# Performance work log

Hardware: AMD Instinct MI355X
Metric: run time of the kernel (lower is better)

The kernel has to match this reference:

```python
import jax, jax.numpy as jnp
from jax import lax
import numpy as np

B, S, D = 32, 2048, 512

def setup_inputs() -> dict:
    key = jax.random.key(0)
    ks = jax.random.split(key, 9)
    inv = 1.0 / np.sqrt(D).astype(np.float32)
    return {
        "query": jax.random.normal(ks[0], (B, 1, D), jnp.float32),
        "value": jax.random.normal(ks[1], (B, S, D), jnp.float32),
        "last_alignment_energy": jax.random.uniform(ks[2], (B, S), jnp.float32),
        "conv_w": jax.random.normal(ks[3], (D, 1, 3), jnp.float32) * 0.1,  # Conv1d(1->D,k=3)
        "conv_b": jax.random.normal(ks[4], (D,), jnp.float32) * 0.01,
        "w_q": jax.random.normal(ks[5], (D, D), jnp.float32) * inv,  # applied as x @ w_q
        "w_v": jax.random.normal(ks[6], (D, D), jnp.float32) * inv,
        "bias": jax.random.uniform(ks[7], (D,), jnp.float32, minval=-0.1, maxval=0.1),
        "score_w": jax.random.normal(ks[8], (D,), jnp.float32) * inv,  # score_proj weight (out=1)
        "score_b": jnp.zeros((), jnp.float32),
    }


def reference(query, value, last_alignment_energy, conv_w, conv_b, w_q, w_v, bias, score_w, score_b):
    # location features: Conv1d(1->D, k=3, pad=1) over the previous alignment
    loc = lax.conv_general_dilated(
        last_alignment_energy[:, None, :], conv_w,
        window_strides=(1,), padding=[(1, 1)],
        dimension_numbers=("NCH", "OIH", "NCH"))  # [B, D, S]
    loc = jnp.transpose(loc, (0, 2, 1)) + conv_b  # [B, S, D]

    # additive attention energy: tanh(Wq q + Wv v + loc + b) @ score_w
    hidden = jnp.tanh(query @ w_q + value @ w_v + loc + bias)  # [B, S, D] (query broadcasts over S)
    scores = hidden @ score_w + score_b                          # [B, S]
    align = jax.nn.softmax(scores, axis=-1)                      # [B, S]

    # context = align^T V
    context = jnp.einsum("bs,bsd->bd", align, value)             # [B, D]
    return context, align
```

## Files before the change

### kernel.cpp

```cpp
#include <hip/hip_runtime.h>
#include <hip/hip_bf16.h>

#define B_ 32
#define S_ 2048
#define D_ 512
#define M_ (B_*S_)

typedef __bf16 bf16x8 __attribute__((ext_vector_type(8)));
typedef float  f32x4  __attribute__((ext_vector_type(4)));

__device__ __forceinline__ float tanh_fast(float x){
  float e2 = __expf(2.f * x);
  return 1.f - 2.f * __builtin_amdgcn_rcpf(e2 + 1.f);
}

__global__ void k_reorder_wv(const float* __restrict__ wv,
                             unsigned short* __restrict__ wvr){
  int frag = blockIdx.x;
  int lane = threadIdx.x;
  int ks = frag >> 5, nt = frag & 31;
  int k0 = ks*32 + (lane>>4)*8;
  int d  = nt*16 + (lane&15);
  bf16x8 t;
  #pragma unroll
  for (int j=0;j<8;++j) t[j] = (__bf16)wv[(k0+j)*D_ + d];
  *reinterpret_cast<uint4*>(wvr + ((size_t)frag*64 + lane)*8) =
      __builtin_bit_cast(uint4, t);
}

__global__ void k_qproj(const float* __restrict__ q,
                        const float* __restrict__ wq,
                        const float* __restrict__ bias,
                        float* __restrict__ qp){
  int b  = blockIdx.y;
  int t  = threadIdx.x;
  int dl = t & 127, eg = t >> 7;
  int d  = blockIdx.x*128 + dl;
  __shared__ float qs[D_];
  __shared__ float red[4][128];
  for (int e=t; e<D_; e+=512) qs[e] = q[b*D_+e];
  __syncthreads();
  float acc = 0.f;
  #pragma unroll 8
  for (int i=0;i<128;++i){
    int e = eg*128 + i;
    acc = fmaf(qs[e], wq[(size_t)e*D_+d], acc);
  }
  red[eg][dl] = acc;
  __syncthreads();
  if (eg == 0)
    qp[b*D_+d] = red[0][dl]+red[1][dl]+red[2][dl]+red[3][dl] + bias[d];
}

__launch_bounds__(256, 2)
__global__ void k_energy(const float* __restrict__ value,
                         const unsigned short* __restrict__ wvr,
                         const float* __restrict__ qp,
                         const float* __restrict__ energy,
                         const float* __restrict__ conv_w,
                         const float* __restrict__ conv_b,
                         const float* __restrict__ score_w,
                         float* __restrict__ scores){
  const int t    = threadIdx.x;
  const int wave = t >> 6;
  const int lane = t & 63;
  const int quad = lane >> 4;
  const int lm   = lane & 15;
  const int row0 = blockIdx.x * 64;
  const int b    = row0 >> 11;
  const int s0   = row0 & (S_-1);

  __shared__ __align__(16) unsigned short As[2][4][64][8];

  const int sr  = t >> 2;
  const int so  = t & 3;
  const float* gA = value + (size_t)(row0+sr)*D_ + so*8;
  unsigned short* wA = &As[0][sr>>4][so*16 + (sr&15)][0];

  f32x4 acc[4][8];
  #pragma unroll
  for (int mt=0;mt<4;++mt)
    #pragma unroll
    for (int nt=0;nt<8;++nt)
      acc[mt][nt] = (f32x4){0.f,0.f,0.f,0.f};

  const unsigned short* bP = wvr + ((size_t)(wave*8)*64 + lane)*8;

  {
    f32x4 p0 = *reinterpret_cast<const f32x4*>(gA);
    f32x4 p1 = *reinterpret_cast<const f32x4*>(gA+4);
    bf16x8 tt;
    tt[0]=(__bf16)p0[0]; tt[1]=(__bf16)p0[1]; tt[2]=(__bf16)p0[2]; tt[3]=(__bf16)p0[3];
    tt[4]=(__bf16)p1[0]; tt[5]=(__bf16)p1[1]; tt[6]=(__bf16)p1[2]; tt[7]=(__bf16)p1[3];
    *reinterpret_cast<uint4*>(wA) = __builtin_bit_cast(uint4, tt);
  }
  __syncthreads();

  for (int kc=0; kc<16; ++kc){
    const int buf = kc & 1;
    f32x4 n0, n1;
    if (kc < 15){
      n0 = *reinterpret_cast<const f32x4*>(gA + (kc+1)*32);
      n1 = *reinterpret_cast<const f32x4*>(gA + (kc+1)*32 + 4);
    }
    bf16x8 a[4];
    #pragma unroll
    for (int mt=0;mt<4;++mt)
      a[mt] = *reinterpret_cast<const bf16x8*>(&As[buf][mt][lane][0]);
    bf16x8 bfr[8];
    #pragma unroll
    for (int ntl=0;ntl<8;++ntl)
      bfr[ntl] = __builtin_bit_cast(bf16x8,
        *reinterpret_cast<const uint4*>(bP + (size_t)(kc*32+ntl)*64*8));
    #pragma unroll
    for (int ntl=0;ntl<8;++ntl)
      #pragma unroll
      for (int mt=0;mt<4;++mt)
        acc[mt][ntl] = __builtin_amdgcn_mfma_f32_16x16x32_bf16(a[mt], bfr[ntl], acc[mt][ntl], 0,0,0);
    if (kc < 15){
      bf16x8 tt;
      tt[0]=(__bf16)n0[0]; tt[1]=(__bf16)n0[1]; tt[2]=(__bf16)n0[2]; tt[3]=(__bf16)n0[3];
      tt[4]=(__bf16)n1[0]; tt[5]=(__bf16)n1[1]; tt[6]=(__bf16)n1[2]; tt[7]=(__bf16)n1[3];
      *reinterpret_cast<uint4*>(wA + (buf^1)*2048) = __builtin_bit_cast(uint4, tt);
    }
    __syncthreads();
  }

  float sw[8], c0[8], c1[8], c2[8], cb[8], qv[8];
  #pragma unroll
  for (int ntl=0; ntl<8; ++ntl){
    int d = wave*128 + ntl*16 + lm;
    sw[ntl] = score_w[d];
    c0[ntl] = conv_w[d*3+0];
    c1[ntl] = conv_w[d*3+1];
    c2[ntl] = conv_w[d*3+2];
    cb[ntl] = conv_b[d];
    qv[ntl] = qp[b*D_+d];
  }
  float* red = (float*)&As[0][0][0][0];
  const float* eB = energy + b*S_;
  #pragma unroll
  for (int mt=0; mt<4; ++mt){
    #pragma unroll
    for (int r=0;r<4;++r){
      int sl = mt*16 + quad*4 + r;
      int s  = s0 + sl;
      float em1 = (s > 0)    ? eB[s-1] : 0.f;
      float e0  =              eB[s];
      float ep1 = (s < S_-1) ? eB[s+1] : 0.f;
      float p = 0.f;
      #pragma unroll
      for (int ntl=0; ntl<8; ++ntl){
        float h = acc[mt][ntl][r] + qv[ntl]
                + fmaf(c0[ntl],em1, fmaf(c1[ntl],e0, fmaf(c2[ntl],ep1, cb[ntl])));
        p = fmaf(sw[ntl], tanh_fast(h), p);
      }
      #pragma unroll
      for (int m=1; m<16; m<<=1) p += __shfl_xor(p, m, 64);
      if (lm == 0) red[wave*64 + sl] = p;
    }
  }
  __syncthreads();
  if (t < 64)
    scores[row0 + t] = red[t] + red[64+t] + red[128+t] + red[192+t];
}

__global__ void k_softmax(const float* __restrict__ sp,
                          const float* __restrict__ score_b,
                          float* __restrict__ out_align){
  int b = blockIdx.x, t = threadIdx.x;
  int lane = t & 63, wid = t >> 6;
  float sb = score_b[0];
  float v[8], mx = -3.4e38f;
  #pragma unroll
  for (int i=0;i<8;++i){
    float sc = sp[b*S_ + t + i*256] + sb;
    v[i] = sc;
    mx = fmaxf(mx, sc);
  }
  __shared__ float red[4], red2[4];
  #pragma unroll
  for (int m=1;m<64;m<<=1) mx = fmaxf(mx, __shfl_xor(mx, m, 64));
  if (lane==0) red[wid] = mx;
  __syncthreads();
  mx = fmaxf(fmaxf(red[0],red[1]), fmaxf(red[2],red[3]));
  float sum = 0.f;
  #pragma unroll
  for (int i=0;i<8;++i){ v[i] = __expf(v[i]-mx); sum += v[i]; }
  #pragma unroll
  for (int m=1;m<64;m<<=1) sum += __shfl_xor(sum, m, 64);
  if (lane==0) red2[wid] = sum;
  __syncthreads();
  sum = red2[0]+red2[1]+red2[2]+red2[3];
  float inv = 1.f/sum;
  #pragma unroll
  for (int i=0;i<8;++i) out_align[b*S_ + t + i*256] = v[i]*inv;
}

__global__ void k_ctx_part(const float* __restrict__ value,
                           const float* __restrict__ align,
                           float* __restrict__ cpart){
  int b = blockIdx.y, sc = blockIdx.x;
  int t = threadIdx.x;
  int r = t >> 7;
  int c = (t & 127) * 4;
  f32x4 acc = (f32x4){0.f,0.f,0.f,0.f};
  for (int i=0;i<64;++i){
    int s = sc*128 + i*2 + r;
    float al = align[b*S_+s];
    f32x4 v = *reinterpret_cast<const f32x4*>(value + ((size_t)(b*S_+s))*D_ + c);
    acc += al * v;
  }
  __shared__ float lred[2][D_];
  #pragma unroll
  for (int j=0;j<4;++j) lred[r][c+j] = acc[j];
  __syncthreads();
  if (r == 0){
    #pragma unroll
    for (int j=0;j<4;++j)
      cpart[((size_t)(b*16+sc))*D_ + c + j] = lred[0][c+j] + lred[1][c+j];
  }
}

__global__ void k_ctx_reduce(const float* __restrict__ cpart,
                             float* __restrict__ out_ctx){
  int idx = blockIdx.x*256 + threadIdx.x;
  int b = idx >> 9, d = idx & 511;
  float s = 0.f;
  #pragma unroll
  for (int j=0;j<16;++j) s += cpart[((size_t)(b*16+j))*D_ + d];
  out_ctx[idx] = s;
}

extern "C" void kernel_launch(void* const* d_in, const int* in_sizes, int n_in,
                              void* d_out, int out_size, void* d_ws, size_t ws_size,
                              hipStream_t stream){
  const float* query   = (const float*)d_in[0];
  const float* value   = (const float*)d_in[1];
  const float* energy  = (const float*)d_in[2];
  const float* conv_w  = (const float*)d_in[3];
  const float* conv_b  = (const float*)d_in[4];
  const float* w_q     = (const float*)d_in[5];
  const float* w_v     = (const float*)d_in[6];
  const float* bias    = (const float*)d_in[7];
  const float* score_w = (const float*)d_in[8];
  const float* score_b = (const float*)d_in[9];

  char* ws = (char*)d_ws;
  unsigned short* wvr = (unsigned short*)(ws);
  float* qp    = (float*)(ws + (512<<10));
  float* sp    = (float*)(ws + (576<<10));
  float* cpart = (float*)(ws + (832<<10));

  float* out_ctx   = (float*)d_out;
  float* out_align = out_ctx + B_*D_;

  k_reorder_wv<<<dim3(512),      dim3(64),  0, stream>>>(w_v, wvr);
  k_qproj     <<<dim3(4,32),     dim3(512), 0, stream>>>(query, w_q, bias, qp);
  k_energy    <<<dim3(M_/64),    dim3(256), 0, stream>>>(value, wvr, qp, energy,
                                                         conv_w, conv_b, score_w, sp);
  k_softmax   <<<dim3(B_),       dim3(256), 0, stream>>>(sp, score_b, out_align);
  k_ctx_part  <<<dim3(16,B_),    dim3(256), 0, stream>>>(value, out_align, cpart);
  k_ctx_reduce<<<dim3(B_*D_/256),dim3(256), 0, stream>>>(cpart, out_ctx);
}
```

Before: 287.3 us.

## Retile energy GEMM to 128x256 blocks with LDS-staged weights and split columns

The energy GEMM now gives each block 128 rows and half of the D columns. The two column halves write partial scores that the softmax kernel sums. Weight fragments are staged into LDS with global_load_lds and shared by the waves, instead of each wave reading them from global memory. This raises reuse of both A and B tiles, at the cost of value rows being read twice, once per column half. The ctx partial kernel now uses 512 threads with four row groups, which adds parallelism in the context reduction.

Measured after the change: 289.0 us. About the same (+0.6%).

```diff
diff --git a/kernel.cpp b/kernel.cpp
--- a/kernel.cpp
+++ b/kernel.cpp
@@ -12,6 +12,19 @@
 __device__ __forceinline__ float tanh_fast(float x){
   float e2 = __expf(2.f * x);
   return 1.f - 2.f * __builtin_amdgcn_rcpf(e2 + 1.f);
+}
+
+__device__ __forceinline__ void gl_lds16(const void* g, void* l){
+  __builtin_amdgcn_global_load_lds(
+      (const __attribute__((address_space(1))) unsigned int*)g,
+      (__attribute__((address_space(3))) unsigned int*)l, 16, 0, 0);
+}
+
+__device__ __forceinline__ bf16x8 cvt8(f32x4 a, f32x4 b){
+  bf16x8 t;
+  t[0]=(__bf16)a[0]; t[1]=(__bf16)a[1]; t[2]=(__bf16)a[2]; t[3]=(__bf16)a[3];
+  t[4]=(__bf16)b[0]; t[5]=(__bf16)b[1]; t[6]=(__bf16)b[2]; t[7]=(__bf16)b[3];
+  return t;
 }
 
 __global__ void k_reorder_wv(const float* __restrict__ wv,
@@ -60,22 +73,28 @@
                          const float* __restrict__ conv_w,
                          const float* __restrict__ conv_b,
                          const float* __restrict__ score_w,
-                         float* __restrict__ scores){
+                         float* __restrict__ scores_part){
   const int t    = threadIdx.x;
   const int wave = t >> 6;
   const int lane = t & 63;
   const int quad = lane >> 4;
   const int lm   = lane & 15;
-  const int row0 = blockIdx.x * 64;
+  const int wh   = wave & 1;
+  const int wc   = wave >> 1;
+
+  const int rowtile = blockIdx.x >> 1;
+  const int colh    = blockIdx.x & 1;
+  const int row0 = rowtile * 128;
   const int b    = row0 >> 11;
   const int s0   = row0 & (S_-1);
 
-  __shared__ __align__(16) unsigned short As[2][4][64][8];
-
-  const int sr  = t >> 2;
-  const int so  = t & 3;
-  const float* gA = value + (size_t)(row0+sr)*D_ + so*8;
-  unsigned short* wA = &As[0][sr>>4][so*16 + (sr&15)][0];
+  __shared__ __align__(16) unsigned short As[2][4096];
+  __shared__ __align__(16) unsigned short Bs[2][8192];
+
+  const int bmt = t >> 6, bo = (t >> 4) & 3;
+  const int blm = t & 15;
+  const float* gA1 = value + (size_t)(row0 + bmt*16 + blm)*D_ + bo*8;
+  const float* gA2 = gA1 + (size_t)64*D_;
 
   f32x4 acc[4][8];
   #pragma unroll
@@ -84,44 +103,57 @@
     for (int nt=0;nt<8;++nt)
       acc[mt][nt] = (f32x4){0.f,0.f,0.f,0.f};
 
-  const unsigned short* bP = wvr + ((size_t)(wave*8)*64 + lane)*8;
-
   {
-    f32x4 p0 = *reinterpret_cast<const f32x4*>(gA);
-    f32x4 p1 = *reinterpret_cast<const f32x4*>(gA+4);
-    bf16x8 tt;
-    tt[0]=(__bf16)p0[0]; tt[1]=(__bf16)p0[1]; tt[2]=(__bf16)p0[2]; tt[3]=(__bf16)p0[3];
-    tt[4]=(__bf16)p1[0]; tt[5]=(__bf16)p1[1]; tt[6]=(__bf16)p1[2]; tt[7]=(__bf16)p1[3];
-    *reinterpret_cast<uint4*>(wA) = __builtin_bit_cast(uint4, tt);
+    #pragma unroll
+    for (int i=0;i<4;++i){
+      int lf = wave*4 + i;
+      int frag = 0*32 + colh*16 + lf;
+      gl_lds16((const char*)wvr + (size_t)frag*1024 + lane*16,
+               (char*)&Bs[0][0] + lf*1024);
+    }
+    f32x4 p0 = *reinterpret_cast<const f32x4*>(gA1);
+    f32x4 p1 = *reinterpret_cast<const f32x4*>(gA1+4);
+    f32x4 p2 = *reinterpret_cast<const f32x4*>(gA2);
+    f32x4 p3 = *reinterpret_cast<const f32x4*>(gA2+4);
+    *reinterpret_cast<uint4*>(&As[0][(size_t)t*8])       = __builtin_bit_cast(uint4, cvt8(p0,p1));
+    *reinterpret_cast<uint4*>(&As[0][(size_t)(t+256)*8]) = __builtin_bit_cast(uint4, cvt8(p2,p3));
   }
   __syncthreads();
 
   for (int kc=0; kc<16; ++kc){
     const int buf = kc & 1;
-    f32x4 n0, n1;
     if (kc < 15){
-      n0 = *reinterpret_cast<const f32x4*>(gA + (kc+1)*32);
-      n1 = *reinterpret_cast<const f32x4*>(gA + (kc+1)*32 + 4);
+      #pragma unroll
+      for (int i=0;i<4;++i){
+        int lf = wave*4 + i;
+        int frag = (kc+1)*32 + colh*16 + lf;
+        gl_lds16((const char*)wvr + (size_t)frag*1024 + lane*16,
+                 (char*)&Bs[buf^1][0] + lf*1024);
+      }
+    }
+    f32x4 n0,n1,n2,n3;
+    if (kc < 15){
+      n0 = *reinterpret_cast<const f32x4*>(gA1 + (kc+1)*32);
+      n1 = *reinterpret_cast<const f32x4*>(gA1 + (kc+1)*32 + 4);
+      n2 = *reinterpret_cast<const f32x4*>(gA2 + (kc+1)*32);
+      n3 = *reinterpret_cast<const f32x4*>(gA2 + (kc+1)*32 + 4);
     }
     bf16x8 a[4];
     #pragma unroll
     for (int mt=0;mt<4;++mt)
-      a[mt] = *reinterpret_cast<const bf16x8*>(&As[buf][mt][lane][0]);
-    bf16x8 bfr[8];
-    #pragma unroll
-    for (int ntl=0;ntl<8;++ntl)
-      bfr[ntl] = __builtin_bit_cast(bf16x8,
-        *reinterpret_cast<const uint4*>(bP + (size_t)(kc*32+ntl)*64*8));
-    #pragma unroll
-    for (int ntl=0;ntl<8;++ntl)
+      a[mt] = *reinterpret_cast<const bf16x8*>(
+                &As[buf][(size_t)(((wh*4+mt)*64 + quad*16 + lm))*8]);
+    #pragma unroll
+    for (int ntl=0;ntl<8;++ntl){
+      bf16x8 bf = *reinterpret_cast<const bf16x8*>(
+                    &Bs[buf][(size_t)((wc*8+ntl)*64 + lane)*8]);
       #pragma unroll
       for (int mt=0;mt<4;++mt)
-        acc[mt][ntl] = __builtin_amdgcn_mfma_f32_16x16x32_bf16(a[mt], bfr[ntl], acc[mt][ntl], 0,0,0);
+        acc[mt][ntl] = __builtin_amdgcn_mfma_f32_16x16x32_bf16(a[mt], bf, acc[mt][ntl], 0,0,0);
+    }
     if (kc < 15){
-      bf16x8 tt;
-      tt[0]=(__bf16)n0[0]; tt[1]=(__bf16)n0[1]; tt[2]=(__bf16)n0[2]; tt[3]=(__bf16)n0[3];
-      tt[4]=(__bf16)n1[0]; tt[5]=(__bf16)n1[1]; tt[6]=(__bf16)n1[2]; tt[7]=(__bf16)n1[3];
-      *reinterpret_cast<uint4*>(wA + (buf^1)*2048) = __builtin_bit_cast(uint4, tt);
+      *reinterpret_cast<uint4*>(&As[buf^1][(size_t)t*8])       = __builtin_bit_cast(uint4, cvt8(n0,n1));
+      *reinterpret_cast<uint4*>(&As[buf^1][(size_t)(t+256)*8]) = __builtin_bit_cast(uint4, cvt8(n2,n3));
     }
     __syncthreads();
   }
@@ -129,7 +161,7 @@
   float sw[8], c0[8], c1[8], c2[8], cb[8], qv[8];
   #pragma unroll
   for (int ntl=0; ntl<8; ++ntl){
-    int d = wave*128 + ntl*16 + lm;
+    int d = colh*256 + wc*128 + ntl*16 + lm;
     sw[ntl] = score_w[d];
     c0[ntl] = conv_w[d*3+0];
     c1[ntl] = conv_w[d*3+1];
@@ -137,13 +169,13 @@
     cb[ntl] = conv_b[d];
     qv[ntl] = qp[b*D_+d];
   }
-  float* red = (float*)&As[0][0][0][0];
+  float* red = (float*)&As[0][0];
   const float* eB = energy + b*S_;
   #pragma unroll
   for (int mt=0; mt<4; ++mt){
     #pragma unroll
     for (int r=0;r<4;++r){
-      int sl = mt*16 + quad*4 + r;
+      int sl = wh*64 + mt*16 + quad*4 + r;
       int s  = s0 + sl;
       float em1 = (s > 0)    ? eB[s-1] : 0.f;
       float e0  =              eB[s];
@@ -157,12 +189,21 @@
       }
       #pragma unroll
       for (int m=1; m<16; m<<=1) p += __shfl_xor(p, m, 64);
-      if (lm == 0) red[wave*64 + sl] = p;
-    }
-  }
-  __syncthreads();
-  if (t < 64)
-    scores[row0 + t] = red[t] + red[64+t] + red[128+t] + red[192+t];
+      if (lm == 0) red[wave*64 + (sl & 63)] = p;
+    }
+  }
+  __syncthreads();
+  if (t < 128){
+    int half = t >> 6;
+    scores_part[colh*M_ + row0 + t] = red[half*1 + (t&63) + 0]
+                                    ;
+  }
+  if (t < 128){
+    int half = t >> 6;
+    float v0 = red[half*64 + (t&63)];
+    float v1 = red[(2+half)*64 + (t&63)];
+    scores_part[colh*M_ + row0 + t] = v0 + v1;
+  }
 }
 
 __global__ void k_softmax(const float* __restrict__ sp,
@@ -174,7 +215,8 @@
   float v[8], mx = -3.4e38f;
   #pragma unroll
   for (int i=0;i<8;++i){
-    float sc = sp[b*S_ + t + i*256] + sb;
+    int s = t + i*256;
+    float sc = sp[b*S_+s] + sp[M_ + b*S_+s] + sb;
     v[i] = sc;
     mx = fmaxf(mx, sc);
   }
@@ -205,20 +247,22 @@
   int r = t >> 7;
   int c = (t & 127) * 4;
   f32x4 acc = (f32x4){0.f,0.f,0.f,0.f};
-  for (int i=0;i<64;++i){
-    int s = sc*128 + i*2 + r;
+  #pragma unroll 8
+  for (int i=0;i<32;++i){
+    int s = sc*128 + i*4 + r;
     float al = align[b*S_+s];
     f32x4 v = *reinterpret_cast<const f32x4*>(value + ((size_t)(b*S_+s))*D_ + c);
     acc += al * v;
   }
-  __shared__ float lred[2][D_];
+  __shared__ float lred[4][D_];
   #pragma unroll
   for (int j=0;j<4;++j) lred[r][c+j] = acc[j];
   __syncthreads();
   if (r == 0){
     #pragma unroll
     for (int j=0;j<4;++j)
-      cpart[((size_t)(b*16+sc))*D_ + c + j] = lred[0][c+j] + lred[1][c+j];
+      cpart[((size_t)(b*16+sc))*D_ + c + j] =
+          lred[0][c+j] + lred[1][c+j] + lred[2][c+j] + lred[3][c+j];
   }
 }
 
@@ -250,16 +294,16 @@
   unsigned short* wvr = (unsigned short*)(ws);
   float* qp    = (float*)(ws + (512<<10));
   float* sp    = (float*)(ws + (576<<10));
-  float* cpart = (float*)(ws + (832<<10));
+  float* cpart = (float*)(ws + (1088<<10));
 
   float* out_ctx   = (float*)d_out;
   float* out_align = out_ctx + B_*D_;
 
   k_reorder_wv<<<dim3(512),      dim3(64),  0, stream>>>(w_v, wvr);
   k_qproj     <<<dim3(4,32),     dim3(512), 0, stream>>>(query, w_q, bias, qp);
-  k_energy    <<<dim3(M_/64),    dim3(256), 0, stream>>>(value, wvr, qp, energy,
+  k_energy    <<<dim3(M_/128*2), dim3(256), 0, stream>>>(value, wvr, qp, energy,
                                                          conv_w, conv_b, score_w, sp);
   k_softmax   <<<dim3(B_),       dim3(256), 0, stream>>>(sp, score_b, out_align);
-  k_ctx_part  <<<dim3(16,B_),    dim3(256), 0, stream>>>(value, out_align, cpart);
+  k_ctx_part  <<<dim3(16,B_),    dim3(512), 0, stream>>>(value, out_align, cpart);
   k_ctx_reduce<<<dim3(B_*D_/256),dim3(256), 0, stream>>>(cpart, out_ctx);
 }
```

## Load A fragments directly into registers and fuse softmax into context kernel

Applied to the files above, without the earlier changes.

The energy GEMM no longer stages value tiles through double-buffered shared memory with a barrier per k-step. Each lane loads its own A fragment from global memory, converts it to bf16 in registers and prefetches the next chunk. Softmax is folded into the context kernel, where each block recomputes the batch max and sum and writes its slice of the alignment, removing one launch and a round trip. The trade-offs are less-coalesced global loads and redundant softmax reductions across blocks.

Result: slower. 310.2 us (+8.0%).

```diff
diff --git a/kernel.cpp b/kernel.cpp
--- a/kernel.cpp
+++ b/kernel.cpp
@@ -12,6 +12,13 @@
 __device__ __forceinline__ float tanh_fast(float x){
   float e2 = __expf(2.f * x);
   return 1.f - 2.f * __builtin_amdgcn_rcpf(e2 + 1.f);
+}
+
+__device__ __forceinline__ bf16x8 cvt8(f32x4 a, f32x4 b){
+  bf16x8 t;
+  t[0]=(__bf16)a[0]; t[1]=(__bf16)a[1]; t[2]=(__bf16)a[2]; t[3]=(__bf16)a[3];
+  t[4]=(__bf16)b[0]; t[5]=(__bf16)b[1]; t[6]=(__bf16)b[2]; t[7]=(__bf16)b[3];
+  return t;
 }
 
 __global__ void k_reorder_wv(const float* __restrict__ wv,
@@ -70,13 +77,6 @@
   const int b    = row0 >> 11;
   const int s0   = row0 & (S_-1);
 
-  __shared__ __align__(16) unsigned short As[2][4][64][8];
-
-  const int sr  = t >> 2;
-  const int so  = t & 3;
-  const float* gA = value + (size_t)(row0+sr)*D_ + so*8;
-  unsigned short* wA = &As[0][sr>>4][so*16 + (sr&15)][0];
-
   f32x4 acc[4][8];
   #pragma unroll
   for (int mt=0;mt<4;++mt)
@@ -84,46 +84,48 @@
     for (int nt=0;nt<8;++nt)
       acc[mt][nt] = (f32x4){0.f,0.f,0.f,0.f};
 
+  const float* aP = value + (size_t)(row0+lm)*D_ + quad*8;
   const unsigned short* bP = wvr + ((size_t)(wave*8)*64 + lane)*8;
 
+  f32x4 aN[4][2];
+  #pragma unroll
+  for (int mt=0;mt<4;++mt){
+    const float* p = aP + (size_t)mt*16*D_;
+    aN[mt][0] = *reinterpret_cast<const f32x4*>(p);
+    aN[mt][1] = *reinterpret_cast<const f32x4*>(p+4);
+  }
+
+  for (int kc=0; kc<15; ++kc){
+    bf16x8 af[4];
+    #pragma unroll
+    for (int mt=0;mt<4;++mt) af[mt] = cvt8(aN[mt][0], aN[mt][1]);
+    #pragma unroll
+    for (int mt=0;mt<4;++mt){
+      const float* p = aP + (size_t)mt*16*D_ + (kc+1)*32;
+      aN[mt][0] = *reinterpret_cast<const f32x4*>(p);
+      aN[mt][1] = *reinterpret_cast<const f32x4*>(p+4);
+    }
+    #pragma unroll
+    for (int ntl=0;ntl<8;++ntl){
+      bf16x8 bf = __builtin_bit_cast(bf16x8,
+        *reinterpret_cast<const uint4*>(bP + (size_t)(kc*32+ntl)*512));
+      #pragma unroll
+      for (int mt=0;mt<4;++mt)
+        acc[mt][ntl] = __builtin_amdgcn_mfma_f32_16x16x32_bf16(af[mt], bf, acc[mt][ntl], 0,0,0);
+    }
+  }
   {
-    f32x4 p0 = *reinterpret_cast<const f32x4*>(gA);
-    f32x4 p1 = *reinterpret_cast<const f32x4*>(gA+4);
-    bf16x8 tt;
-    tt[0]=(__bf16)p0[0]; tt[1]=(__bf16)p0[1]; tt[2]=(__bf16)p0[2]; tt[3]=(__bf16)p0[3];
-    tt[4]=(__bf16)p1[0]; tt[5]=(__bf16)p1[1]; tt[6]=(__bf16)p1[2]; tt[7]=(__bf16)p1[3];
-    *reinterpret_cast<uint4*>(wA) = __builtin_bit_cast(uint4, tt);
-  }
-  __syncthreads();
-
-  for (int kc=0; kc<16; ++kc){
-    const int buf = kc & 1;
-    f32x4 n0, n1;
-    if (kc < 15){
-      n0 = *reinterpret_cast<const f32x4*>(gA + (kc+1)*32);
-      n1 = *reinterpret_cast<const f32x4*>(gA + (kc+1)*32 + 4);
-    }
-    bf16x8 a[4];
-    #pragma unroll
-    for (int mt=0;mt<4;++mt)
-      a[mt] = *reinterpret_cast<const bf16x8*>(&As[buf][mt][lane][0]);
-    bf16x8 bfr[8];
-    #pragma unroll
-    for (int ntl=0;ntl<8;++ntl)
-      bfr[ntl] = __builtin_bit_cast(bf16x8,
-        *reinterpret_cast<const uint4*>(bP + (size_t)(kc*32+ntl)*64*8));
-    #pragma unroll
-    for (int ntl=0;ntl<8;++ntl)
+    bf16x8 af[4];
+    #pragma unroll
+    for (int mt=0;mt<4;++mt) af[mt] = cvt8(aN[mt][0], aN[mt][1]);
+    #pragma unroll
+    for (int ntl=0;ntl<8;++ntl){
+      bf16x8 bf = __builtin_bit_cast(bf16x8,
+        *reinterpret_cast<const uint4*>(bP + (size_t)(15*32+ntl)*512));
       #pragma unroll
       for (int mt=0;mt<4;++mt)
-        acc[mt][ntl] = __builtin_amdgcn_mfma_f32_16x16x32_bf16(a[mt], bfr[ntl], acc[mt][ntl], 0,0,0);
-    if (kc < 15){
-      bf16x8 tt;
-      tt[0]=(__bf16)n0[0]; tt[1]=(__bf16)n0[1]; tt[2]=(__bf16)n0[2]; tt[3]=(__bf16)n0[3];
-      tt[4]=(__bf16)n1[0]; tt[5]=(__bf16)n1[1]; tt[6]=(__bf16)n1[2]; tt[7]=(__bf16)n1[3];
-      *reinterpret_cast<uint4*>(wA + (buf^1)*2048) = __builtin_bit_cast(uint4, tt);
-    }
-    __syncthreads();
+        acc[mt][ntl] = __builtin_amdgcn_mfma_f32_16x16x32_bf16(af[mt], bf, acc[mt][ntl], 0,0,0);
+    }
   }
 
   float sw[8], c0[8], c1[8], c2[8], cb[8], qv[8];
@@ -137,7 +139,7 @@
     cb[ntl] = conv_b[d];
     qv[ntl] = qp[b*D_+d];
   }
-  float* red = (float*)&As[0][0][0][0];
+  __shared__ float red[4][64];
   const float* eB = energy + b*S_;
   #pragma unroll
   for (int mt=0; mt<4; ++mt){
@@ -157,68 +159,76 @@
       }
       #pragma unroll
       for (int m=1; m<16; m<<=1) p += __shfl_xor(p, m, 64);
-      if (lm == 0) red[wave*64 + sl] = p;
+      if (lm == 0) red[wave][sl] = p;
     }
   }
   __syncthreads();
   if (t < 64)
-    scores[row0 + t] = red[t] + red[64+t] + red[128+t] + red[192+t];
-}
-
-__global__ void k_softmax(const float* __restrict__ sp,
-                          const float* __restrict__ score_b,
-                          float* __restrict__ out_align){
-  int b = blockIdx.x, t = threadIdx.x;
-  int lane = t & 63, wid = t >> 6;
-  float sb = score_b[0];
-  float v[8], mx = -3.4e38f;
-  #pragma unroll
-  for (int i=0;i<8;++i){
-    float sc = sp[b*S_ + t + i*256] + sb;
-    v[i] = sc;
-    mx = fmaxf(mx, sc);
-  }
-  __shared__ float red[4], red2[4];
-  #pragma unroll
-  for (int m=1;m<64;m<<=1) mx = fmaxf(mx, __shfl_xor(mx, m, 64));
-  if (lane==0) red[wid] = mx;
-  __syncthreads();
-  mx = fmaxf(fmaxf(red[0],red[1]), fmaxf(red[2],red[3]));
-  float sum = 0.f;
-  #pragma unroll
-  for (int i=0;i<8;++i){ v[i] = __expf(v[i]-mx); sum += v[i]; }
-  #pragma unroll
-  for (int m=1;m<64;m<<=1) sum += __shfl_xor(sum, m, 64);
-  if (lane==0) red2[wid] = sum;
-  __syncthreads();
-  sum = red2[0]+red2[1]+red2[2]+red2[3];
-  float inv = 1.f/sum;
-  #pragma unroll
-  for (int i=0;i<8;++i) out_align[b*S_ + t + i*256] = v[i]*inv;
-}
-
-__global__ void k_ctx_part(const float* __restrict__ value,
-                           const float* __restrict__ align,
-                           float* __restrict__ cpart){
+    scores[row0 + t] = red[0][t] + red[1][t] + red[2][t] + red[3][t];
+}
+
+__launch_bounds__(512)
+__global__ void k_ctx(const float* __restrict__ scores,
+                      const float* __restrict__ value,
+                      float* __restrict__ out_align,
+                      float* __restrict__ cpart){
   int b = blockIdx.y, sc = blockIdx.x;
   int t = threadIdx.x;
+  int lane = t & 63, wid = t >> 6;
+  __shared__ float redm[8], reds[8];
+  __shared__ float als[128];
+
+  float v[4], mx = -3.4e38f;
+  #pragma unroll
+  for (int i=0;i<4;++i){
+    v[i] = scores[b*S_ + t + i*512];
+    mx = fmaxf(mx, v[i]);
+  }
+  #pragma unroll
+  for (int m=1;m<64;m<<=1) mx = fmaxf(mx, __shfl_xor(mx, m, 64));
+  if (lane==0) redm[wid] = mx;
+  __syncthreads();
+  #pragma unroll
+  for (int w=0;w<8;++w) mx = fmaxf(mx, redm[w]);
+  float sum = 0.f;
+  #pragma unroll
+  for (int i=0;i<4;++i) sum += __expf(v[i]-mx);
+  #pragma unroll
+  for (int m=1;m<64;m<<=1) sum += __shfl_xor(sum, m, 64);
+  if (lane==0) reds[wid] = sum;
+  __syncthreads();
+  sum = 0.f;
+  #pragma unroll
+  for (int w=0;w<8;++w) sum += reds[w];
+  float inv = 1.f/sum;
+
+  if (t < 128){
+    float a = __expf(scores[b*S_ + sc*128 + t] - mx) * inv;
+    out_align[b*S_ + sc*128 + t] = a;
+    als[t] = a;
+  }
+  __syncthreads();
+
   int r = t >> 7;
   int c = (t & 127) * 4;
   f32x4 acc = (f32x4){0.f,0.f,0.f,0.f};
-  for (int i=0;i<64;++i){
-    int s = sc*128 + i*2 + r;
-    float al = align[b*S_+s];
-    f32x4 v = *reinterpret_cast<const f32x4*>(value + ((size_t)(b*S_+s))*D_ + c);
-    acc += al * v;
-  }
-  __shared__ float lred[2][D_];
+  #pragma unroll 8
+  for (int i=0;i<32;++i){
+    int sl = i*4 + r;
+    float al = als[sl];
+    f32x4 vv = *reinterpret_cast<const f32x4*>(
+                 value + ((size_t)(b*S_ + sc*128 + sl))*D_ + c);
+    acc += al * vv;
+  }
+  __shared__ float lred[4][D_];
   #pragma unroll
   for (int j=0;j<4;++j) lred[r][c+j] = acc[j];
   __syncthreads();
   if (r == 0){
     #pragma unroll
     for (int j=0;j<4;++j)
-      cpart[((size_t)(b*16+sc))*D_ + c + j] = lred[0][c+j] + lred[1][c+j];
+      cpart[((size_t)(b*16+sc))*D_ + c + j] =
+          lred[0][c+j] + lred[1][c+j] + lred[2][c+j] + lred[3][c+j];
   }
 }
 
@@ -244,13 +254,12 @@
   const float* w_v     = (const float*)d_in[6];
   const float* bias    = (const float*)d_in[7];
   const float* score_w = (const float*)d_in[8];
-  const float* score_b = (const float*)d_in[9];
 
   char* ws = (char*)d_ws;
   unsigned short* wvr = (unsigned short*)(ws);
-  float* qp    = (float*)(ws + (512<<10));
-  float* sp    = (float*)(ws + (576<<10));
-  float* cpart = (float*)(ws + (832<<10));
+  float* qp     = (float*)(ws + (512<<10));
+  float* scores = (float*)(ws + (576<<10));
+  float* cpart  = (float*)(ws + (832<<10));
 
   float* out_ctx   = (float*)d_out;
   float* out_align = out_ctx + B_*D_;
@@ -258,8 +267,7 @@
   k_reorder_wv<<<dim3(512),      dim3(64),  0, stream>>>(w_v, wvr);
   k_qproj     <<<dim3(4,32),     dim3(512), 0, stream>>>(query, w_q, bias, qp);
   k_energy    <<<dim3(M_/64),    dim3(256), 0, stream>>>(value, wvr, qp, energy,
-                                                         conv_w, conv_b, score_w, sp);
-  k_softmax   <<<dim3(B_),       dim3(256), 0, stream>>>(sp, score_b, out_align);
-  k_ctx_part  <<<dim3(16,B_),    dim3(256), 0, stream>>>(value, out_align, cpart);
+                                                         conv_w, conv_b, score_w, scores);
+  k_ctx       <<<dim3(16,B_),    dim3(512), 0, stream>>>(scores, value, out_align, cpart);
   k_ctx_reduce<<<dim3(B_*D_/256),dim3(256), 0, stream>>>(cpart, out_ctx);
 }
```
